# Performance work log

Hardware: AMD Instinct MI355X
Metric: run time of the kernel (lower is better)

## Reference

```python
import jax, jax.numpy as jnp
import numpy as np

N_NODES = 50000
N_EDGES = 1_600_000
D_IN = 128
D_HID = 128
D_OUT = 128


def _linear_init(key, out_dim, in_dim, bias=True):
    k1, k2 = jax.random.split(key)
    bound = 1.0 / np.sqrt(in_dim)
    W = jax.random.uniform(k1, (out_dim, in_dim), jnp.float32, -bound, bound)
    if bias:
        b = jax.random.uniform(k2, (out_dim,), jnp.float32, -bound, bound)
        return W, b
    return W, None


def _leconv_params(key, in_dim, out_dim):
    k1, k2, k3 = jax.random.split(key, 3)
    W1, b1 = _linear_init(k1, out_dim, in_dim, bias=True)   # lin1 (applied to x_j)
    W2, _ = _linear_init(k2, out_dim, in_dim, bias=False)   # lin2 (applied to x_i)
    W3, b3 = _linear_init(k3, out_dim, in_dim, bias=True)   # lin3 (skip on x_i)
    return W1, b1, W2, W3, b3


def setup_inputs() -> dict:
    key = jax.random.key(0)
    kx, ke, kw, k_in, k_mid, k_out = jax.random.split(key, 6)
    x = jax.random.normal(kx, (N_NODES, D_IN), jnp.float32)
    edge_index = jax.random.randint(ke, (2, N_EDGES), 0, N_NODES, dtype=jnp.int32)
    edge_weight = jax.random.uniform(kw, (N_EDGES,), jnp.float32)
    iW1, ib1, iW2, iW3, ib3 = _leconv_params(k_in, D_IN, D_HID)
    mW1, mb1, mW2, mW3, mb3 = _leconv_params(k_mid, D_HID, D_HID)
    oW1, ob1, oW2, oW3, ob3 = _leconv_params(k_out, D_HID, D_OUT)
    return {
        "x": x, "edge_index": edge_index, "edge_weight": edge_weight,
        "in_W1": iW1, "in_b1": ib1, "in_W2": iW2, "in_W3": iW3, "in_b3": ib3,
        "mid_W1": mW1, "mid_b1": mb1, "mid_W2": mW2, "mid_W3": mW3, "mid_b3": mb3,
        "out_W1": oW1, "out_b1": ob1, "out_W2": oW2, "out_W3": oW3, "out_b3": ob3,
        "number_of_layers": 4,
    }


def _leconv(h, src, dst, ew, W1, b1, W2, W3, b3):
    # out_i = sum_{j->i} e_ji * ((W1 x_j + b1) - W2 x_i) + (W3 x_i + b3)
    a = h @ W1.T + b1          # [N, F_out]
    b = h @ W2.T               # [N, F_out]
    msg = ew[:, None] * (a[src] - b[dst])              # [E, F_out]
    agg = jax.ops.segment_sum(msg, dst, num_segments=h.shape[0])
    return agg + h @ W3.T + b3


def _lrelu(x):
    return jnp.where(x >= 0, x, 0.1 * x)


def reference(x, edge_index, edge_weight,
              in_W1, in_b1, in_W2, in_W3, in_b3,
              mid_W1, mid_b1, mid_W2, mid_W3, mid_b3,
              out_W1, out_b1, out_W2, out_W3, out_b3,
              number_of_layers):
    src, dst = edge_index[0], edge_index[1]
    h = _lrelu(_leconv(x, src, dst, edge_weight, in_W1, in_b1, in_W2, in_W3, in_b3))
    for _ in range(number_of_layers - 2):  # shared inner weights, as in the torch module
        h = _lrelu(_leconv(h, src, dst, edge_weight, mid_W1, mid_b1, mid_W2, mid_W3, mid_b3))
    h = _lrelu(_leconv(h, src, dst, edge_weight, out_W1, out_b1, out_W2, out_W3, out_b3))
    return jax.nn.sigmoid(h)
```

## Files before the change

### kernel.cpp

```cpp
#include <hip/hip_runtime.h>
#include <hip/hip_fp16.h>
#include <math.h>

#define D 128
#define CSH 11
#define BSH 7
#define NB_MAX 512
#define NKEY 3584

typedef _Float16 f16;
typedef __attribute__((ext_vector_type(8))) _Float16 f16x8;
typedef __attribute__((ext_vector_type(4))) float f32x4;


__global__ __launch_bounds__(256) void binA_count(
    const int* __restrict__ dst, int* __restrict__ bucketCount, int E)
{
    __shared__ int hist[NB_MAX];
    int tid = threadIdx.x;
    for (int i = tid; i < NB_MAX; i += 256) hist[i] = 0;
    __syncthreads();
    int base = blockIdx.x * 4096;
    for (int i = tid; i < 4096; i += 256) {
        int e = base + i;
        if (e < E) atomicAdd(&hist[dst[e] >> BSH], 1);
    }
    __syncthreads();
    for (int i = tid; i < NB_MAX; i += 256)
        if (hist[i]) atomicAdd(&bucketCount[i], hist[i]);
}

__global__ __launch_bounds__(512) void bucket_scan(
    const int* __restrict__ bucketCount, int* __restrict__ bucketBase,
    int* __restrict__ bucketCursor, int* __restrict__ row_off,
    int NBUC, int E, int N)
{
    __shared__ int wsum[8];
    int tid  = threadIdx.x;
    int lane = tid & 63;
    int wid  = tid >> 6;
    int v = (tid < NBUC) ? bucketCount[tid] : 0;
    int x = v;
    #pragma unroll
    for (int o = 1; o < 64; o <<= 1) { int t = __shfl_up(x, o); if (lane >= o) x += t; }
    if (lane == 63) wsum[wid] = x;
    __syncthreads();
    if (tid < 8) {
        int y = wsum[tid];
        #pragma unroll
        for (int o = 1; o < 8; o <<= 1) { int t = __shfl_up(y, o, 8); if (tid >= o) y += t; }
        wsum[tid] = y;
    }
    __syncthreads();
    int excl = (wid ? wsum[wid - 1] : 0) + x - v;
    if (tid <= NBUC) {
        bucketBase[tid] = excl;
        if (tid < NBUC) bucketCursor[tid] = excl;
    }
    if (tid == 0) row_off[N] = E;
}

__global__ __launch_bounds__(256) void binA_scatter(
    const int* __restrict__ src, const int* __restrict__ dst,
    const float* __restrict__ ew, int* __restrict__ bucketCursor,
    int2* __restrict__ binned, int E)
{
    __shared__ int hist[NB_MAX], off[NB_MAX], cbase[NB_MAX];
    int tid = threadIdx.x;
    for (int i = tid; i < NB_MAX; i += 256) { hist[i] = 0; off[i] = 0; }
    __syncthreads();
    int base = blockIdx.x * 4096;
    for (int i = tid; i < 4096; i += 256) {
        int e = base + i;
        if (e < E) atomicAdd(&hist[dst[e] >> BSH], 1);
    }
    __syncthreads();
    for (int i = tid; i < NB_MAX; i += 256)
        if (hist[i]) cbase[i] = atomicAdd(&bucketCursor[i], hist[i]);
    __syncthreads();
    for (int i = tid; i < 4096; i += 256) {
        int e = base + i;
        if (e < E) {
            int d = dst[e];
            int b = d >> BSH;
            int pos = cbase[b] + atomicAdd(&off[b], 1);
            binned[pos] = make_int2(src[e] | (d << 16), __float_as_int(ew[e]));
        }
    }
}

__global__ __launch_bounds__(512) void binB_kernel(
    const int2* __restrict__ binned, const int* __restrict__ bucketBase,
    int2* __restrict__ edge_s, int* __restrict__ row_off,
    float* __restrict__ sdeg, int N, int nchunk)
{
    __shared__ int hist[NKEY];
    __shared__ int cur[NKEY];
    __shared__ float sdl[128];
    __shared__ int wsum[8];

    int b    = blockIdx.x;
    int tid  = threadIdx.x;
    int ebeg = bucketBase[b], eend = bucketBase[b + 1];
    int node0 = b << BSH;
    int nib   = min(128, N - node0);

    for (int i = tid; i < NKEY; i += 512) hist[i] = 0;
    if (tid < 128) sdl[tid] = 0.f;
    __syncthreads();

    for (int e = ebeg + tid; e < eend; e += 512) {
        int2 ed = binned[e];
        int s  = ed.x & 0xffff;
        int dl = (int)(((unsigned)ed.x) >> 16) - node0;
        int ch = s >> CSH;
        atomicAdd(&hist[dl * nchunk + ch], 1);
        atomicAdd(&sdl[dl], __int_as_float(ed.y));
    }
    __syncthreads();

    int base_i = tid * 7;
    int v[7];
    int tot = 0;
    #pragma unroll
    for (int j = 0; j < 7; ++j) { v[j] = hist[base_i + j]; tot += v[j]; }
    int lane = tid & 63, wid = tid >> 6;
    int x = tot;
    #pragma unroll
    for (int o = 1; o < 64; o <<= 1) { int t = __shfl_up(x, o); if (lane >= o) x += t; }
    if (lane == 63) wsum[wid] = x;
    __syncthreads();
    if (tid < 8) {
        int y = wsum[tid];
        #pragma unroll
        for (int o = 1; o < 8; o <<= 1) { int t = __shfl_up(y, o, 8); if (tid >= o) y += t; }
        wsum[tid] = y;
    }
    __syncthreads();
    int p = (wid ? wsum[wid - 1] : 0) + x - tot;
    #pragma unroll
    for (int j = 0; j < 7; ++j) { cur[base_i + j] = p; p += v[j]; }
    __syncthreads();

    for (int dl = tid; dl < nib; dl += 512) {
        row_off[node0 + dl] = ebeg + cur[dl * nchunk];
        sdeg[node0 + dl]    = sdl[dl];
    }
    __syncthreads();

    for (int e = ebeg + tid; e < eend; e += 512) {
        int2 ed = binned[e];
        int s  = ed.x & 0xffff;
        int dl = (int)(((unsigned)ed.x) >> 16) - node0;
        int ch = s >> CSH;
        int pos = ebeg + atomicAdd(&cur[dl * nchunk + ch], 1);
        edge_s[pos] = make_int2(s, ed.y);
    }
}

__global__ __launch_bounds__(256) void pack_kernel(
    const float* __restrict__ W1, const float* __restrict__ W2,
    const float* __restrict__ W3, f16* __restrict__ Wp)
{
    int idx = blockIdx.x * 256 + threadIdx.x;
    if (idx >= 6144) return;
    int lane = idx & 63;
    int t    = idx >> 6;
    int ks   = t & 3;
    int mot  = t >> 2;
    int m    = mot >> 3;
    int ot   = mot & 7;
    const float* W = (m == 0) ? W1 : (m == 1) ? W2 : W3;
    int o  = ot * 16 + (lane & 15);
    int kb = ks * 32 + (lane >> 4) * 8;
    f16x8 hi, lo;
    #pragma unroll
    for (int j = 0; j < 8; ++j) {
        float v = W[(size_t)o * D + kb + j];
        f16 hh = (f16)v;
        hi[j] = hh;
        lo[j] = (f16)(v - (float)hh);
    }
    size_t base = (size_t)ks * 24576 + (size_t)mot * 1024 + (size_t)lane * 8;
    *(f16x8*)&Wp[base]       = hi;
    *(f16x8*)&Wp[base + 512] = lo;
}


__global__ __launch_bounds__(256, 2) void gemm_kernel(
    const float* __restrict__ in, const f16* __restrict__ Wp,
    const float* __restrict__ b1, const float* __restrict__ b3,
    const float* __restrict__ sdeg, float* __restrict__ aF,
    float* __restrict__ base_out, int N, int ntiles, int gridb)
{
    int tid  = threadIdx.x;
    int lane = tid & 63;
    int wid  = tid >> 6;
    int col  = lane & 15;
    int g    = lane >> 4;

    f16x8 w[3][2][4][2];
    #pragma unroll
    for (int m = 0; m < 3; ++m)
        #pragma unroll
        for (int oti = 0; oti < 2; ++oti) {
            int mot = m * 8 + wid * 2 + oti;
            #pragma unroll
            for (int ks = 0; ks < 4; ++ks) {
                const f16* p = Wp + (size_t)ks * 24576 + (size_t)mot * 1024 + (size_t)lane * 8;
                w[m][oti][ks][0] = *(const f16x8*)p;
                w[m][oti][ks][1] = *(const f16x8*)(p + 512);
            }
        }

    float bi1[2], bi3[2];
    #pragma unroll
    for (int oti = 0; oti < 2; ++oti) {
        int o = (wid * 2 + oti) * 16 + col;
        bi1[oti] = b1[o];
        bi3[oti] = b3[o];
    }

    for (int t = blockIdx.x; t < ntiles; t += gridb) {
        int n0   = t * 16;
        int nrow = n0 + col;

        f32x4 acc[3][2];
        #pragma unroll
        for (int m = 0; m < 3; ++m)
            #pragma unroll
            for (int oti = 0; oti < 2; ++oti)
                acc[m][oti] = (f32x4){0.f, 0.f, 0.f, 0.f};

        #pragma unroll
        for (int ks = 0; ks < 4; ++ks) {
            float av[8];
            if (nrow < N) {
                float4 a0 = *(const float4*)&in[(size_t)nrow * D + ks * 32 + g * 8];
                float4 a1 = *(const float4*)&in[(size_t)nrow * D + ks * 32 + g * 8 + 4];
                av[0] = a0.x; av[1] = a0.y; av[2] = a0.z; av[3] = a0.w;
                av[4] = a1.x; av[5] = a1.y; av[6] = a1.z; av[7] = a1.w;
            } else {
                #pragma unroll
                for (int j = 0; j < 8; ++j) av[j] = 0.f;
            }
            f16x8 ahi, alo;
            #pragma unroll
            for (int j = 0; j < 8; ++j) {
                f16 hh = (f16)av[j];
                ahi[j] = hh;
                alo[j] = (f16)(av[j] - (float)hh);
            }
            #pragma unroll
            for (int m = 0; m < 3; ++m)
                #pragma unroll
                for (int oti = 0; oti < 2; ++oti) {
                    acc[m][oti] = __builtin_amdgcn_mfma_f32_16x16x32_f16(ahi, w[m][oti][ks][0], acc[m][oti], 0, 0, 0);
                    acc[m][oti] = __builtin_amdgcn_mfma_f32_16x16x32_f16(alo, w[m][oti][ks][0], acc[m][oti], 0, 0, 0);
                    acc[m][oti] = __builtin_amdgcn_mfma_f32_16x16x32_f16(ahi, w[m][oti][ks][1], acc[m][oti], 0, 0, 0);
                }
        }

        #pragma unroll
        for (int oti = 0; oti < 2; ++oti) {
            int o = (wid * 2 + oti) * 16 + col;
            #pragma unroll
            for (int r = 0; r < 4; ++r) {
                int node = n0 + g * 4 + r;
                if (node < N) {
                    float sv   = sdeg[node];
                    float aval = acc[0][oti][r] + bi1[oti];
                    float bval = acc[2][oti][r] + bi3[oti] - sv * acc[1][oti][r];
                    aF[(size_t)node * D + o]       = aval;
                    base_out[(size_t)node * D + o] = bval;
                }
            }
        }
    }
}


__global__ __launch_bounds__(256) void agg_kernel(
    const float* __restrict__ aF, const float* __restrict__ base,
    const int* __restrict__ row_off, const int2* __restrict__ edge_s,
    float* __restrict__ out, int N, int last)
{
    int lane = threadIdx.x & 63;
    int wid  = threadIdx.x >> 6;
    int node = blockIdx.x * 4 + wid;
    if (node >= N) return;
    int half = lane >> 5;
    int fl   = (lane & 31) * 4;

    float4 acc = make_float4(0.f, 0.f, 0.f, 0.f);
    int beg = row_off[node], end = row_off[node + 1];

    int e = beg + half;
    for (; e + 14 < end; e += 16) {
        int2 m[8];
        #pragma unroll
        for (int i = 0; i < 8; ++i) m[i] = edge_s[e + i * 2];
        float4 v[8];
        #pragma unroll
        for (int i = 0; i < 8; ++i)
            v[i] = *(const float4*)&aF[(size_t)m[i].x * D + fl];
        #pragma unroll
        for (int i = 0; i < 8; ++i) {
            float wgt = __int_as_float(m[i].y);
            acc.x = fmaf(wgt, v[i].x, acc.x);
            acc.y = fmaf(wgt, v[i].y, acc.y);
            acc.z = fmaf(wgt, v[i].z, acc.z);
            acc.w = fmaf(wgt, v[i].w, acc.w);
        }
    }
    for (; e + 6 < end; e += 8) {
        int2 m[4];
        #pragma unroll
        for (int i = 0; i < 4; ++i) m[i] = edge_s[e + i * 2];
        float4 v[4];
        #pragma unroll
        for (int i = 0; i < 4; ++i)
            v[i] = *(const float4*)&aF[(size_t)m[i].x * D + fl];
        #pragma unroll
        for (int i = 0; i < 4; ++i) {
            float wgt = __int_as_float(m[i].y);
            acc.x = fmaf(wgt, v[i].x, acc.x);
            acc.y = fmaf(wgt, v[i].y, acc.y);
            acc.z = fmaf(wgt, v[i].z, acc.z);
            acc.w = fmaf(wgt, v[i].w, acc.w);
        }
    }
    for (; e < end; e += 2) {
        int2 m = edge_s[e];
        float4 v = *(const float4*)&aF[(size_t)m.x * D + fl];
        float wgt = __int_as_float(m.y);
        acc.x = fmaf(wgt, v.x, acc.x);
        acc.y = fmaf(wgt, v.y, acc.y);
        acc.z = fmaf(wgt, v.z, acc.z);
        acc.w = fmaf(wgt, v.w, acc.w);
    }

    acc.x += __shfl_xor(acc.x, 32);
    acc.y += __shfl_xor(acc.y, 32);
    acc.z += __shfl_xor(acc.z, 32);
    acc.w += __shfl_xor(acc.w, 32);

    if (half == 0) {
        float4 b = *(const float4*)&base[(size_t)node * D + fl];
        float r0 = acc.x + b.x, r1 = acc.y + b.y;
        float r2 = acc.z + b.z, r3 = acc.w + b.w;
        r0 = r0 >= 0.f ? r0 : 0.1f * r0;
        r1 = r1 >= 0.f ? r1 : 0.1f * r1;
        r2 = r2 >= 0.f ? r2 : 0.1f * r2;
        r3 = r3 >= 0.f ? r3 : 0.1f * r3;
        if (last) {
            r0 = 1.f / (1.f + __expf(-r0));
            r1 = 1.f / (1.f + __expf(-r1));
            r2 = 1.f / (1.f + __expf(-r2));
            r3 = 1.f / (1.f + __expf(-r3));
        }
        *(float4*)&out[(size_t)node * D + fl] = make_float4(r0, r1, r2, r3);
    }
}


extern "C" void kernel_launch(void* const* d_in, const int* in_sizes, int n_in,
                              void* d_out, int out_size, void* d_ws, size_t ws_size,
                              hipStream_t stream) {
    const float* x   = (const float*)d_in[0];
    const int*   ei  = (const int*)d_in[1];
    const float* ew  = (const float*)d_in[2];
    const float* iW1 = (const float*)d_in[3];
    const float* ib1 = (const float*)d_in[4];
    const float* iW2 = (const float*)d_in[5];
    const float* iW3 = (const float*)d_in[6];
    const float* ib3 = (const float*)d_in[7];
    const float* mW1 = (const float*)d_in[8];
    const float* mb1 = (const float*)d_in[9];
    const float* mW2 = (const float*)d_in[10];
    const float* mW3 = (const float*)d_in[11];
    const float* mb3 = (const float*)d_in[12];
    const float* oW1 = (const float*)d_in[13];
    const float* ob1 = (const float*)d_in[14];
    const float* oW2 = (const float*)d_in[15];
    const float* oW3 = (const float*)d_in[16];
    const float* ob3 = (const float*)d_in[17];

    int N = in_sizes[0] / D;
    int E = in_sizes[2];
    const int* src = ei;
    const int* dst = ei + E;
    int nchunk = (N + (1 << CSH) - 1) >> CSH;
    int NBUC   = (N + (1 << BSH) - 1) >> BSH;

    char* wsp = (char*)d_ws;
    size_t off = 0;
    auto alloc = [&](size_t bytes) -> void* {
        void* p = wsp + off;
        off += (bytes + 255) & ~(size_t)255;
        return p;
    };
    float* h       = (float*)alloc((size_t)N * D * 4);
    float* base    = (float*)alloc((size_t)N * D * 4);
    float* aF      = (float*)alloc((size_t)N * D * 4);
    float* sdeg    = (float*)alloc((size_t)N * 4);
    int*   row_off = (int*)alloc((size_t)(N + 1) * 4);
    int2*  edge_s  = (int2*)alloc((size_t)E * 8);
    int*   bucketCount  = (int*)alloc((size_t)(NBUC + 1) * 4);
    int*   bucketBase   = (int*)alloc((size_t)(NBUC + 1) * 4);
    int*   bucketCursor = (int*)alloc((size_t)(NBUC + 1) * 4);
    f16*   Wp       = (f16*)alloc((size_t)3 * 98304 * 2);

    int2* binned = (int2*)h;

    hipMemsetAsync(bucketCount, 0, (size_t)(NBUC + 1) * 4, stream);

    int ablocks  = (N + 3) / 4;
    int ntiles   = (N + 15) / 16;
    int gridb    = 512;
    int abblocks = (E + 4095) / 4096;

    pack_kernel<<<24, 256, 0, stream>>>(iW1, iW2, iW3, Wp);
    pack_kernel<<<24, 256, 0, stream>>>(mW1, mW2, mW3, Wp + 98304);
    pack_kernel<<<24, 256, 0, stream>>>(oW1, oW2, oW3, Wp + 2 * 98304);

    binA_count<<<abblocks, 256, 0, stream>>>(dst, bucketCount, E);
    bucket_scan<<<1, 512, 0, stream>>>(bucketCount, bucketBase, bucketCursor,
                                       row_off, NBUC, E, N);
    binA_scatter<<<abblocks, 256, 0, stream>>>(src, dst, ew, bucketCursor,
                                               binned, E);
    binB_kernel<<<NBUC, 512, 0, stream>>>(binned, bucketBase, edge_s,
                                          row_off, sdeg, N, nchunk);

    gemm_kernel<<<gridb, 256, 0, stream>>>(x, Wp, ib1, ib3, sdeg, aF, base, N, ntiles, gridb);
    agg_kernel<<<ablocks, 256, 0, stream>>>(aF, base, row_off, edge_s, h, N, 0);
    for (int l = 0; l < 2; ++l) {
        gemm_kernel<<<gridb, 256, 0, stream>>>(h, Wp + 98304, mb1, mb3, sdeg, aF, base, N, ntiles, gridb);
        agg_kernel<<<ablocks, 256, 0, stream>>>(aF, base, row_off, edge_s, h, N, 0);
    }
    gemm_kernel<<<gridb, 256, 0, stream>>>(h, Wp + 2 * 98304, ob1, ob3, sdeg, aF, base, N, ntiles, gridb);
    agg_kernel<<<ablocks, 256, 0, stream>>>(aF, base, row_off, edge_s, (float*)d_out, N, 1);
}
```

Baseline: 630.5 us.

## Split GEMM output tiles across block pairs to cut registers and raise occupancy

Each wave now handles one 16-wide output tile instead of two. The output columns are split between pairs of blocks, which halves the preloaded weight registers and the accumulators per thread. Launch bounds go from 2 to 3 blocks per SM and the grid grows from 512 to 1536, aiming for more waves in flight to hide the latency of the input loads. In exchange, every input row tile is loaded and split into hi/lo f16 by two blocks instead of one, doubling input reads and conversion work.

```diff
diff --git a/kernel.cpp b/kernel.cpp
--- a/kernel.cpp
+++ b/kernel.cpp
@@ -187,7 +187,7 @@
 }
 
 
-__global__ __launch_bounds__(256, 2) void gemm_kernel(
+__global__ __launch_bounds__(256, 3) void gemm_kernel(
     const float* __restrict__ in, const f16* __restrict__ Wp,
     const float* __restrict__ b1, const float* __restrict__ b3,
     const float* __restrict__ sdeg, float* __restrict__ aF,
@@ -198,39 +198,31 @@
     int wid  = tid >> 6;
     int col  = lane & 15;
     int g    = lane >> 4;
-
-    f16x8 w[3][2][4][2];
-    #pragma unroll
-    for (int m = 0; m < 3; ++m)
-        #pragma unroll
-        for (int oti = 0; oti < 2; ++oti) {
-            int mot = m * 8 + wid * 2 + oti;
-            #pragma unroll
-            for (int ks = 0; ks < 4; ++ks) {
-                const f16* p = Wp + (size_t)ks * 24576 + (size_t)mot * 1024 + (size_t)lane * 8;
-                w[m][oti][ks][0] = *(const f16x8*)p;
-                w[m][oti][ks][1] = *(const f16x8*)(p + 512);
-            }
-        }
-
-    float bi1[2], bi3[2];
-    #pragma unroll
-    for (int oti = 0; oti < 2; ++oti) {
-        int o = (wid * 2 + oti) * 16 + col;
-        bi1[oti] = b1[o];
-        bi3[oti] = b3[o];
-    }
-
-    for (int t = blockIdx.x; t < ntiles; t += gridb) {
+    int ot   = (blockIdx.x & 1) * 4 + wid;
+
+    f16x8 w[3][4][2];
+    #pragma unroll
+    for (int m = 0; m < 3; ++m) {
+        int mot = m * 8 + ot;
+        #pragma unroll
+        for (int ks = 0; ks < 4; ++ks) {
+            const f16* p = Wp + (size_t)ks * 24576 + (size_t)mot * 1024 + (size_t)lane * 8;
+            w[m][ks][0] = *(const f16x8*)p;
+            w[m][ks][1] = *(const f16x8*)(p + 512);
+        }
+    }
+
+    int o   = ot * 16 + col;
+    float bi1 = b1[o];
+    float bi3 = b3[o];
+
+    for (int t = blockIdx.x >> 1; t < ntiles; t += (gridb >> 1)) {
         int n0   = t * 16;
         int nrow = n0 + col;
 
-        f32x4 acc[3][2];
-        #pragma unroll
-        for (int m = 0; m < 3; ++m)
-            #pragma unroll
-            for (int oti = 0; oti < 2; ++oti)
-                acc[m][oti] = (f32x4){0.f, 0.f, 0.f, 0.f};
+        f32x4 acc[3];
+        #pragma unroll
+        for (int m = 0; m < 3; ++m) acc[m] = (f32x4){0.f, 0.f, 0.f, 0.f};
 
         #pragma unroll
         for (int ks = 0; ks < 4; ++ks) {
@@ -252,28 +244,22 @@
                 alo[j] = (f16)(av[j] - (float)hh);
             }
             #pragma unroll
-            for (int m = 0; m < 3; ++m)
-                #pragma unroll
-                for (int oti = 0; oti < 2; ++oti) {
-                    acc[m][oti] = __builtin_amdgcn_mfma_f32_16x16x32_f16(ahi, w[m][oti][ks][0], acc[m][oti], 0, 0, 0);
-                    acc[m][oti] = __builtin_amdgcn_mfma_f32_16x16x32_f16(alo, w[m][oti][ks][0], acc[m][oti], 0, 0, 0);
-                    acc[m][oti] = __builtin_amdgcn_mfma_f32_16x16x32_f16(ahi, w[m][oti][ks][1], acc[m][oti], 0, 0, 0);
-                }
-        }
-
-        #pragma unroll
-        for (int oti = 0; oti < 2; ++oti) {
-            int o = (wid * 2 + oti) * 16 + col;
-            #pragma unroll
-            for (int r = 0; r < 4; ++r) {
-                int node = n0 + g * 4 + r;
-                if (node < N) {
-                    float sv   = sdeg[node];
-                    float aval = acc[0][oti][r] + bi1[oti];
-                    float bval = acc[2][oti][r] + bi3[oti] - sv * acc[1][oti][r];
-                    aF[(size_t)node * D + o]       = aval;
-                    base_out[(size_t)node * D + o] = bval;
-                }
+            for (int m = 0; m < 3; ++m) {
+                acc[m] = __builtin_amdgcn_mfma_f32_16x16x32_f16(ahi, w[m][ks][0], acc[m], 0, 0, 0);
+                acc[m] = __builtin_amdgcn_mfma_f32_16x16x32_f16(alo, w[m][ks][0], acc[m], 0, 0, 0);
+                acc[m] = __builtin_amdgcn_mfma_f32_16x16x32_f16(ahi, w[m][ks][1], acc[m], 0, 0, 0);
+            }
+        }
+
+        #pragma unroll
+        for (int r = 0; r < 4; ++r) {
+            int node = n0 + g * 4 + r;
+            if (node < N) {
+                float sv   = sdeg[node];
+                float aval = acc[0][r] + bi1;
+                float bval = acc[2][r] + bi3 - sv * acc[1][r];
+                aF[(size_t)node * D + o]       = aval;
+                base_out[(size_t)node * D + o] = bval;
             }
         }
     }
@@ -417,7 +403,7 @@
 
     int ablocks  = (N + 3) / 4;
     int ntiles   = (N + 15) / 16;
-    int gridb    = 512;
+    int gridb    = 1536;
     int abblocks = (E + 4095) / 4096;
 
     pack_kernel<<<24, 256, 0, stream>>>(iW1, iW2, iW3, Wp);
```

Result: no change. 641.8 us (+1.8%).
